# Performance work log

Hardware: AMD Instinct MI355X
Metric: run time of the kernel (lower is better)

The kernel has to match this reference:

```python
import jax, jax.numpy as jnp
import numpy as np

B, S, D = 2, 2048, 2048
H, KVH = 32, 8
HD = D // H            # 64
G = H // KVH           # 4 kv groups
SCALE = 1.0 / np.sqrt(HD)


def setup_inputs() -> dict:
    key = jax.random.key(0)
    k1, k2, k3, k4, k5 = jax.random.split(key, 5)
    hidden_states = jax.random.normal(k1, (B, S, D), dtype=jnp.float32)
    Wq = jax.random.normal(k2, (D, H * HD), dtype=jnp.float32) * 0.02
    Wk = jax.random.normal(k3, (D, KVH * HD), dtype=jnp.float32) * 0.02
    Wv = jax.random.normal(k4, (D, KVH * HD), dtype=jnp.float32) * 0.02
    Wo = jax.random.normal(k5, (H * HD, D), dtype=jnp.float32) * 0.02
    return {"hidden_states": hidden_states, "Wq": Wq, "Wk": Wk, "Wv": Wv, "Wo": Wo}


def reference(hidden_states, Wq, Wk, Wv, Wo):
    B_, S_, _ = hidden_states.shape
    q = (hidden_states @ Wq).reshape(B_, S_, H, HD).transpose(0, 2, 1, 3)      # [B,H,S,HD]
    k = (hidden_states @ Wk).reshape(B_, S_, KVH, HD).transpose(0, 2, 1, 3)    # [B,KVH,S,HD]
    v = (hidden_states @ Wv).reshape(B_, S_, KVH, HD).transpose(0, 2, 1, 3)
    # repeat_interleave over head dim: kv head g serves q heads [g*G, (g+1)*G)
    k = jnp.repeat(k, G, axis=1)  # [B,H,S,HD]
    v = jnp.repeat(v, G, axis=1)
    scores = jnp.einsum('bhqd,bhkd->bhqk', q, k) * SCALE
    probs = jax.nn.softmax(scores.astype(jnp.float32), axis=-1).astype(q.dtype)
    # dropout is identity in eval mode
    out = jnp.einsum('bhqk,bhkd->bhqd', probs, v)             # [B,H,S,HD]
    out = out.transpose(0, 2, 1, 3).reshape(B_, S_, H * HD)   # [B,S,D]
    return out @ Wo
```

## Files before the change

kernel.cpp:

```cpp
#include <hip/hip_runtime.h>
#include <hip/hip_bf16.h>

typedef unsigned short u16;
typedef __attribute__((ext_vector_type(8))) short short8;
typedef __attribute__((ext_vector_type(4))) float f32x4;
typedef __attribute__((ext_vector_type(16))) float f32x16;
typedef __attribute__((ext_vector_type(4))) unsigned short u16x4;
typedef __attribute__((ext_vector_type(4))) int int4v;

#define S_LEN 2048
#define NH 32
#define NKV 8
#define QSCALE 0.18033688011112042f
#define PSHIFT 14.0f

__device__ __forceinline__ float fexp2(float x) { return __builtin_amdgcn_exp2f(x); }

__device__ __forceinline__ u16 f2bf(float f) {
  unsigned int u = __builtin_bit_cast(unsigned int, f);
  u += 0x7fffu + ((u >> 16) & 1u);
  return (u16)(u >> 16);
}

__device__ __forceinline__ unsigned int pk2bf(float a, float b) {
  float2 t; t.x = a; t.y = b;
  __hip_bfloat162 h = __float22bfloat162_rn(t);
  unsigned int r;
  __builtin_memcpy(&r, &h, 4);
  return r;
}

__device__ __forceinline__ void async16(const void* g, void* l) {
  __builtin_amdgcn_global_load_lds(
      (__attribute__((address_space(1))) void*)g,
      (__attribute__((address_space(3))) void*)l, 16, 0, 0);
}

__device__ __forceinline__ short8 mk_pf(unsigned a, unsigned b, unsigned c, unsigned d) {
  int4v t; t.x = (int)a; t.y = (int)b; t.z = (int)c; t.w = (int)d;
  return __builtin_bit_cast(short8, t);
}

__global__ __launch_bounds__(256) void prep_kernel(const float* __restrict__ X,
                                                   const float* __restrict__ Wq,
                                                   const float* __restrict__ Wk,
                                                   const float* __restrict__ Wv,
                                                   const float* __restrict__ Wo,
                                                   u16* __restrict__ Xb,
                                                   u16* __restrict__ Wqt,
                                                   u16* __restrict__ Wkt,
                                                   u16* __restrict__ Wvt,
                                                   u16* __restrict__ Wot) {
  __shared__ float tile[32][33];
  int bx = blockIdx.x, tid = threadIdx.x;
  if (bx < 8192) {
    int idx = bx * 256 + tid;
    float4 v = ((const float4*)X)[idx];
    u16x4 o;
    o.x = f2bf(v.x); o.y = f2bf(v.y); o.z = f2bf(v.z); o.w = f2bf(v.w);
    *(u16x4*)&Xb[(size_t)idx * 4] = o;
    return;
  }
  const float* in; u16* out; int N, bi;
  if (bx < 12288)      { bi = bx - 8192;  in = Wq; out = Wqt; N = 2048; }
  else if (bx < 13312) { bi = bx - 12288; in = Wk; out = Wkt; N = 512; }
  else if (bx < 14336) { bi = bx - 13312; in = Wv; out = Wvt; N = 512; }
  else                 { bi = bx - 14336; in = Wo; out = Wot; N = 2048; }
  const int K = 2048;
  int nbx = N >> 5;
  int n0 = (bi % nbx) * 32, k0 = (bi / nbx) * 32;
  int tx = tid & 31, ty = tid >> 5;
#pragma unroll
  for (int i = 0; i < 32; i += 8)
    tile[ty + i][tx] = in[(size_t)(k0 + ty + i) * N + n0 + tx];
  __syncthreads();
#pragma unroll
  for (int i = 0; i < 32; i += 8)
    out[(size_t)(n0 + ty + i) * K + k0 + tx] = f2bf(tile[tx][ty + i]);
}

__global__ __launch_bounds__(256) void gemm_qkv(const u16* __restrict__ A,
                                                const u16* __restrict__ Wqt,
                                                const u16* __restrict__ Wkvt,
                                                u16* __restrict__ Qb,
                                                u16* __restrict__ KVb) {
  __shared__ u16 la0[4096], la1[4096], lb0[4096], lb1[4096];
  int tid = threadIdx.x, bx = blockIdx.x;
  int mode, bm, bn;
  const u16* Bt;
  if (bx < 512) { mode = 0; bm = bx >> 4; bn = bx & 15; Bt = Wqt; }
  else          { mode = 1; int b2 = bx - 512; bm = b2 >> 3; bn = b2 & 7; Bt = Wkvt; }
  const int K = 2048;
  int w = tid >> 6, lane = tid & 63, qd = lane >> 4, ln = lane & 15;
  int wm = w >> 1, wn = w & 1;
  f32x4 acc[4][4];
#pragma unroll
  for (int i = 0; i < 4; ++i)
#pragma unroll
    for (int j = 0; j < 4; ++j) acc[i][j] = {0.f, 0.f, 0.f, 0.f};

  const u16* Ab = A + (size_t)bm * 128 * K;
  const u16* Bb = Bt + (size_t)bn * 128 * K;
  int row0 = tid >> 2, c0 = tid & 3;
  int g0 = c0 ^ (row0 & 3) ^ ((row0 >> 2) & 3);
  int s1 = tid + 256, row1 = s1 >> 2, c1 = s1 & 3;
  int g1 = c1 ^ (row1 & 3) ^ ((row1 >> 2) & 3);
  int pat = (ln & 3) ^ ((ln >> 2) & 3);
  int goff = (qd ^ pat) * 8;
  const u16* pa0 = Ab + (size_t)row0 * K + g0 * 8;
  const u16* pa1 = Ab + (size_t)row1 * K + g1 * 8;
  const u16* pb0 = Bb + (size_t)row0 * K + g0 * 8;
  const u16* pb1 = Bb + (size_t)row1 * K + g1 * 8;

#define QKV_STAGE(LA, LB, OFS)                      \
  async16(pa0 + (OFS), &LA[tid * 8]);               \
  async16(pa1 + (OFS), &LA[2048 + tid * 8]);        \
  async16(pb0 + (OFS), &LB[tid * 8]);               \
  async16(pb1 + (OFS), &LB[2048 + tid * 8]);

#define QKV_COMPUTE(LA, LB)                                                        \
  {                                                                                \
    short8 af[4], bf[4];                                                           \
    _Pragma("unroll") for (int i = 0; i < 4; ++i)                                  \
        af[i] = *(const short8*)&LA[(wm * 64 + i * 16 + ln) * 32 + goff];          \
    _Pragma("unroll") for (int j = 0; j < 4; ++j)                                  \
        bf[j] = *(const short8*)&LB[(wn * 64 + j * 16 + ln) * 32 + goff];          \
    __builtin_amdgcn_s_setprio(1);                                                 \
    _Pragma("unroll") for (int i = 0; i < 4; ++i)                                  \
      _Pragma("unroll") for (int j = 0; j < 4; ++j)                                \
        acc[i][j] =                                                                \
            __builtin_amdgcn_mfma_f32_16x16x32_bf16(af[i], bf[j], acc[i][j], 0, 0, 0); \
    __builtin_amdgcn_s_setprio(0);                                                 \
  }

  QKV_STAGE(la0, lb0, 0);
  __syncthreads();

  for (int kt = 0; kt < K; kt += 64) {
    QKV_STAGE(la1, lb1, kt + 32);
    QKV_COMPUTE(la0, lb0);
    __syncthreads();
    if (kt + 64 < K) { QKV_STAGE(la0, lb0, kt + 64); }
    QKV_COMPUTE(la1, lb1);
    __syncthreads();
  }
#undef QKV_STAGE
#undef QKV_COMPUTE

#pragma unroll
  for (int i = 0; i < 4; ++i)
#pragma unroll
    for (int r = 0; r < 4; ++r) {
      int m = bm * 128 + wm * 64 + i * 16 + qd * 4 + r;
      int b = m >> 11, s = m & 2047;
#pragma unroll
      for (int j = 0; j < 4; ++j) {
        int n = bn * 128 + wn * 64 + j * 16 + ln;
        float v = acc[i][j][r];
        int hh = n >> 6, hd = n & 63;
        if (mode == 0) {
          Qb[(((size_t)(b * NH + hh)) * S_LEN + s) * 64 + hd] = f2bf(v * QSCALE);
        } else {
          if (hh < 8)
            KVb[(((size_t)(b * NKV + hh)) * S_LEN + s) * 64 + hd] = f2bf(v);
          else
            KVb[2097152 + (((size_t)(b * NKV + (hh - 8))) * 64 + hd) * S_LEN + s] = f2bf(v);
        }
      }
    }
}

__global__ __launch_bounds__(256) void gemm_out(const u16* __restrict__ A,
                                                const u16* __restrict__ Bt,
                                                float* __restrict__ outp) {
  __shared__ u16 la0[4096], la1[4096], lb0[4096], lb1[4096];
  const int K = 2048, N = 2048;
  int tid = threadIdx.x;
  int bm = blockIdx.x >> 4, bn = blockIdx.x & 15;
  int w = tid >> 6, lane = tid & 63, qd = lane >> 4, ln = lane & 15;
  int wm = w >> 1, wn = w & 1;
  f32x4 acc[4][4];
#pragma unroll
  for (int i = 0; i < 4; ++i)
#pragma unroll
    for (int j = 0; j < 4; ++j) acc[i][j] = {0.f, 0.f, 0.f, 0.f};

  const u16* Ab = A + (size_t)bm * 128 * K;
  const u16* Bb = Bt + (size_t)bn * 128 * K;
  int row0 = tid >> 2, c0 = tid & 3;
  int g0 = c0 ^ (row0 & 3) ^ ((row0 >> 2) & 3);
  int s1 = tid + 256, row1 = s1 >> 2, c1 = s1 & 3;
  int g1 = c1 ^ (row1 & 3) ^ ((row1 >> 2) & 3);
  int pat = (ln & 3) ^ ((ln >> 2) & 3);
  int goff = (qd ^ pat) * 8;
  const u16* pa0 = Ab + (size_t)row0 * K + g0 * 8;
  const u16* pa1 = Ab + (size_t)row1 * K + g1 * 8;
  const u16* pb0 = Bb + (size_t)row0 * K + g0 * 8;
  const u16* pb1 = Bb + (size_t)row1 * K + g1 * 8;

#define OUT_STAGE(LA, LB, OFS)                      \
  async16(pa0 + (OFS), &LA[tid * 8]);               \
  async16(pa1 + (OFS), &LA[2048 + tid * 8]);        \
  async16(pb0 + (OFS), &LB[tid * 8]);               \
  async16(pb1 + (OFS), &LB[2048 + tid * 8]);

#define OUT_COMPUTE(LA, LB)                                                        \
  {                                                                                \
    short8 af[4], bf[4];                                                           \
    _Pragma("unroll") for (int i = 0; i < 4; ++i)                                  \
        af[i] = *(const short8*)&LA[(wm * 64 + i * 16 + ln) * 32 + goff];          \
    _Pragma("unroll") for (int j = 0; j < 4; ++j)                                  \
        bf[j] = *(const short8*)&LB[(wn * 64 + j * 16 + ln) * 32 + goff];          \
    __builtin_amdgcn_s_setprio(1);                                                 \
    _Pragma("unroll") for (int i = 0; i < 4; ++i)                                  \
      _Pragma("unroll") for (int j = 0; j < 4; ++j)                                \
        acc[i][j] =                                                                \
            __builtin_amdgcn_mfma_f32_16x16x32_bf16(af[i], bf[j], acc[i][j], 0, 0, 0); \
    __builtin_amdgcn_s_setprio(0);                                                 \
  }

  OUT_STAGE(la0, lb0, 0);
  __syncthreads();

  for (int kt = 0; kt < K; kt += 64) {
    OUT_STAGE(la1, lb1, kt + 32);
    OUT_COMPUTE(la0, lb0);
    __syncthreads();
    if (kt + 64 < K) { OUT_STAGE(la0, lb0, kt + 64); }
    OUT_COMPUTE(la1, lb1);
    __syncthreads();
  }
#undef OUT_STAGE
#undef OUT_COMPUTE

#pragma unroll
  for (int i = 0; i < 4; ++i)
#pragma unroll
    for (int r = 0; r < 4; ++r) {
      int m = bm * 128 + wm * 64 + i * 16 + qd * 4 + r;
#pragma unroll
      for (int j = 0; j < 4; ++j) {
        int n = bn * 128 + wn * 64 + j * 16 + ln;
        outp[(size_t)m * N + n] = acc[i][j][r];
      }
    }
}

__global__ __launch_bounds__(256, 2) void attn_kernel(const u16* __restrict__ Q,
                                                      const u16* __restrict__ K,
                                                      const u16* __restrict__ VT,
                                                      u16* __restrict__ Ao) {
  __shared__ u16 sh[16384];
  int tid = threadIdx.x;
  int w = tid >> 6, lane = tid & 63;
  int l31 = lane & 31, l5 = lane >> 5;
  int qt = blockIdx.x & 7, bh = blockIdx.x >> 3;
  int b = bh >> 5, h = bh & 31, g = h >> 2;
  const u16* gQ = Q + ((size_t)bh * S_LEN + qt * 256) * 64;
  const u16* gK = K + (size_t)(b * NKV + g) * S_LEN * 64;
  const u16* gV = VT + (size_t)(b * NKV + g) * 64 * S_LEN;

  int p7 = l31 & 7;

  int s0 = tid, r0 = s0 >> 3, c0 = s0 & 7, gg0 = c0 ^ (r0 & 7);
  int s1 = tid + 256, r1 = s1 >> 3, c1 = s1 & 7, gg1 = c1 ^ (r1 & 7);

#pragma unroll
  for (int k = 0; k < 8; ++k) {
    int s = tid + k * 256;
    int q = s >> 3, c = s & 7, gg = c ^ (q & 7);
    async16(gQ + (size_t)q * 64 + gg * 8, &sh[s * 8]);
  }
  __syncthreads();
  short8 qf[2][4];
#pragma unroll
  for (int qg = 0; qg < 2; ++qg) {
    int qrow = w * 64 + qg * 32 + l31;
#pragma unroll
    for (int ks = 0; ks < 4; ++ks)
      qf[qg][ks] = *(const short8*)&sh[qrow * 64 + ((ks * 2 + l5) ^ p7) * 8];
  }
  __syncthreads();

  async16(gK + (size_t)r0 * 64 + gg0 * 8, &sh[s0 * 8]);
  async16(gK + (size_t)r1 * 64 + gg1 * 8, &sh[s1 * 8]);
  async16(gV + (size_t)r0 * S_LEN + gg0 * 8, &sh[8192 + s0 * 8]);
  async16(gV + (size_t)r1 * S_LEN + gg1 * 8, &sh[8192 + s1 * 8]);
  __syncthreads();

  const f32x16 psh16 = {-PSHIFT, -PSHIFT, -PSHIFT, -PSHIFT, -PSHIFT, -PSHIFT,
                        -PSHIFT, -PSHIFT, -PSHIFT, -PSHIFT, -PSHIFT, -PSHIFT,
                        -PSHIFT, -PSHIFT, -PSHIFT, -PSHIFT};
  f32x16 accA0, accA1, accB0, accB1;
#pragma unroll
  for (int t = 0; t < 16; ++t) { accA0[t] = 0.f; accA1[t] = 0.f; accB0[t] = 0.f; accB1[t] = 0.f; }
  float liA = 0.f, liB = 0.f;

#define SOFTMAX32(SC, LI, PF0, PF1)                                              \
  short8 PF0, PF1;                                                               \
  {                                                                              \
    float p[16];                                                                 \
    _Pragma("unroll") for (int t = 0; t < 16; ++t) p[t] = fexp2(SC[t]);          \
    _Pragma("unroll") for (int t = 0; t < 16; t += 4)                            \
        LI += (p[t] + p[t + 1]) + (p[t + 2] + p[t + 3]);                         \
    unsigned W[8];                                                               \
    _Pragma("unroll") for (int t = 0; t < 8; ++t) W[t] = pk2bf(p[2 * t], p[2 * t + 1]); \
    auto ra = __builtin_amdgcn_permlane32_swap((int)W[0], (int)W[2], false, false); \
    auto rb = __builtin_amdgcn_permlane32_swap((int)W[1], (int)W[3], false, false); \
    auto rc = __builtin_amdgcn_permlane32_swap((int)W[4], (int)W[6], false, false); \
    auto rd = __builtin_amdgcn_permlane32_swap((int)W[5], (int)W[7], false, false); \
    PF0 = mk_pf((unsigned)ra[0], (unsigned)rb[0], (unsigned)ra[1], (unsigned)rb[1]); \
    PF1 = mk_pf((unsigned)rc[0], (unsigned)rd[0], (unsigned)rc[1], (unsigned)rd[1]); \
  }

  for (int c = 0; c < 32; ++c) {
    int cur = c & 1;
    if (c < 31) {
      int nb = cur ^ 1, cn = c + 1;
      async16(gK + (size_t)(cn * 64 + r0) * 64 + gg0 * 8, &sh[nb * 4096 + s0 * 8]);
      async16(gK + (size_t)(cn * 64 + r1) * 64 + gg1 * 8, &sh[nb * 4096 + s1 * 8]);
      async16(gV + (size_t)r0 * S_LEN + cn * 64 + gg0 * 8, &sh[8192 + nb * 4096 + s0 * 8]);
      async16(gV + (size_t)r1 * S_LEN + cn * 64 + gg1 * 8, &sh[8192 + nb * 4096 + s1 * 8]);
    }
    const u16* kb = &sh[cur * 4096];
    const u16* vb = &sh[8192 + cur * 4096];

#pragma unroll
    for (int kblk = 0; kblk < 2; ++kblk) {
      f32x16 scA = psh16, scB = psh16;
      __builtin_amdgcn_s_setprio(1);
#pragma unroll
      for (int ks = 0; ks < 4; ++ks) {
        short8 kf = *(const short8*)&kb[(kblk * 32 + l31) * 64 + ((ks * 2 + l5) ^ p7) * 8];
        scA = __builtin_amdgcn_mfma_f32_32x32x16_bf16(kf, qf[0][ks], scA, 0, 0, 0);
        scB = __builtin_amdgcn_mfma_f32_32x32x16_bf16(kf, qf[1][ks], scB, 0, 0, 0);
      }
      __builtin_amdgcn_s_setprio(0);

      SOFTMAX32(scA, liA, pfA0, pfA1)
      SOFTMAX32(scB, liB, pfB0, pfB1)

      __builtin_amdgcn_s_setprio(1);
#pragma unroll
      for (int hb = 0; hb < 2; ++hb) {
        short8 vf = *(const short8*)&vb[(hb * 32 + l31) * 64 + ((kblk * 4 + l5) ^ p7) * 8];
        if (hb == 0) {
          accA0 = __builtin_amdgcn_mfma_f32_32x32x16_bf16(vf, pfA0, accA0, 0, 0, 0);
          accB0 = __builtin_amdgcn_mfma_f32_32x32x16_bf16(vf, pfB0, accB0, 0, 0, 0);
        } else {
          accA1 = __builtin_amdgcn_mfma_f32_32x32x16_bf16(vf, pfA0, accA1, 0, 0, 0);
          accB1 = __builtin_amdgcn_mfma_f32_32x32x16_bf16(vf, pfB0, accB1, 0, 0, 0);
        }
      }
#pragma unroll
      for (int hb = 0; hb < 2; ++hb) {
        short8 vf = *(const short8*)&vb[(hb * 32 + l31) * 64 + ((kblk * 4 + 2 + l5) ^ p7) * 8];
        if (hb == 0) {
          accA0 = __builtin_amdgcn_mfma_f32_32x32x16_bf16(vf, pfA1, accA0, 0, 0, 0);
          accB0 = __builtin_amdgcn_mfma_f32_32x32x16_bf16(vf, pfB1, accB0, 0, 0, 0);
        } else {
          accA1 = __builtin_amdgcn_mfma_f32_32x32x16_bf16(vf, pfA1, accA1, 0, 0, 0);
          accB1 = __builtin_amdgcn_mfma_f32_32x32x16_bf16(vf, pfB1, accB1, 0, 0, 0);
        }
      }
      __builtin_amdgcn_s_setprio(0);
    }
    __syncthreads();
  }
#undef SOFTMAX32

  {
    float l = liA + __shfl_xor(liA, 32);
    float inv = 1.f / l;
    int q = qt * 256 + w * 64 + l31;
    size_t base = ((size_t)b * S_LEN + q) * 2048 + h * 64;
#pragma unroll
    for (int rq = 0; rq < 4; ++rq) {
      u16x4 o0, o1;
#pragma unroll
      for (int rr = 0; rr < 4; ++rr) {
        o0[rr] = f2bf(accA0[rq * 4 + rr] * inv);
        o1[rr] = f2bf(accA1[rq * 4 + rr] * inv);
      }
      *(u16x4*)&Ao[base + rq * 8 + l5 * 4] = o0;
      *(u16x4*)&Ao[base + 32 + rq * 8 + l5 * 4] = o1;
    }
  }
  {
    float l = liB + __shfl_xor(liB, 32);
    float inv = 1.f / l;
    int q = qt * 256 + w * 64 + 32 + l31;
    size_t base = ((size_t)b * S_LEN + q) * 2048 + h * 64;
#pragma unroll
    for (int rq = 0; rq < 4; ++rq) {
      u16x4 o0, o1;
#pragma unroll
      for (int rr = 0; rr < 4; ++rr) {
        o0[rr] = f2bf(accB0[rq * 4 + rr] * inv);
        o1[rr] = f2bf(accB1[rq * 4 + rr] * inv);
      }
      *(u16x4*)&Ao[base + rq * 8 + l5 * 4] = o0;
      *(u16x4*)&Ao[base + 32 + rq * 8 + l5 * 4] = o1;
    }
  }
}

extern "C" void kernel_launch(void* const* d_in, const int* in_sizes, int n_in,
                              void* d_out, int out_size, void* d_ws, size_t ws_size,
                              hipStream_t stream) {
  const float* X  = (const float*)d_in[0];
  const float* Wq = (const float*)d_in[1];
  const float* Wk = (const float*)d_in[2];
  const float* Wv = (const float*)d_in[3];
  const float* Wo = (const float*)d_in[4];
  char* ws = (char*)d_ws;
  u16* Xb  = (u16*)(ws);
  u16* Wqt = (u16*)(ws + 16777216);
  u16* Wkt = (u16*)(ws + 25165824);
  u16* Wvt = (u16*)(ws + 27262976);
  u16* Wot = (u16*)(ws + 29360128);
  u16* Qb  = (u16*)(ws + 37748736);
  u16* Kb  = (u16*)(ws + 54525952);
  u16* VTb = (u16*)(ws + 58720256);
  u16* Ab  = (u16*)(ws + 62914560);
  float* out = (float*)d_out;

  prep_kernel<<<18432, 256, 0, stream>>>(X, Wq, Wk, Wv, Wo, Xb, Wqt, Wkt, Wvt, Wot);
  gemm_qkv<<<768, 256, 0, stream>>>(Xb, Wqt, Wkt, Qb, Kb);
  attn_kernel<<<512, 256, 0, stream>>>(Qb, Kb, VTb, Ab);
  gemm_out<<<512, 256, 0, stream>>>(Ab, Wot, out);
}
```

Before: 304.0 us.

## Triple-buffer LDS stages in QKV and output GEMMs with explicit vmcnt waits

Replaces the double-buffered K loop in both projection GEMMs with a three-stage LDS ring. Two tiles are kept in flight, and partial s_waitcnt vmcnt counts with raw barriers replace the full __syncthreads. The aim is to hide global-load latency behind MFMA work, since only the oldest stage now has to land before compute. The cost is 50% more shared memory per block, which may reduce occupancy, and hand-tuned waitcnt values that depend on the async16 instruction count per stage.

```diff
diff --git a/kernel.cpp b/kernel.cpp
--- a/kernel.cpp
+++ b/kernel.cpp
@@ -84,7 +84,8 @@
                                                 const u16* __restrict__ Wkvt,
                                                 u16* __restrict__ Qb,
                                                 u16* __restrict__ KVb) {
-  __shared__ u16 la0[4096], la1[4096], lb0[4096], lb1[4096];
+  __shared__ u16 la0[4096], la1[4096], la2[4096];
+  __shared__ u16 lb0[4096], lb1[4096], lb2[4096];
   int tid = threadIdx.x, bx = blockIdx.x;
   int mode, bm, bn;
   const u16* Bt;
@@ -133,19 +134,38 @@
     __builtin_amdgcn_s_setprio(0);                                                 \
   }
 
+#define QKV_STEP(CA, CB, SA, SB, SOFS, VM)                          \
+  asm volatile("s_waitcnt lgkmcnt(0)" ::: "memory");                \
+  __builtin_amdgcn_s_barrier();                                     \
+  QKV_STAGE(SA, SB, SOFS);                                          \
+  asm volatile("s_waitcnt vmcnt(" #VM ")" ::: "memory");            \
+  __builtin_amdgcn_s_barrier();                                     \
+  QKV_COMPUTE(CA, CB);
+
+#define QKV_STEP_T(CA, CB, VM)                                      \
+  asm volatile("s_waitcnt lgkmcnt(0)" ::: "memory");                \
+  __builtin_amdgcn_s_barrier();                                     \
+  asm volatile("s_waitcnt vmcnt(" #VM ")" ::: "memory");            \
+  __builtin_amdgcn_s_barrier();                                     \
+  QKV_COMPUTE(CA, CB);
+
   QKV_STAGE(la0, lb0, 0);
-  __syncthreads();
-
-  for (int kt = 0; kt < K; kt += 64) {
-    QKV_STAGE(la1, lb1, kt + 32);
-    QKV_COMPUTE(la0, lb0);
-    __syncthreads();
-    if (kt + 64 < K) { QKV_STAGE(la0, lb0, kt + 64); }
-    QKV_COMPUTE(la1, lb1);
-    __syncthreads();
-  }
+  QKV_STAGE(la1, lb1, 32);
+
+  for (int t3 = 0; t3 < 60; t3 += 3) {
+    int ofs = t3 * 32;
+    QKV_STEP(la0, lb0, la2, lb2, ofs + 64, 8);
+    QKV_STEP(la1, lb1, la0, lb0, ofs + 96, 8);
+    QKV_STEP(la2, lb2, la1, lb1, ofs + 128, 8);
+  }
+  QKV_STEP(la0, lb0, la2, lb2, 1984, 8);
+  QKV_STEP(la1, lb1, la0, lb0, 2016, 8);
+  QKV_STEP_T(la2, lb2, 4);
+  QKV_STEP_T(la0, lb0, 0);
 #undef QKV_STAGE
 #undef QKV_COMPUTE
+#undef QKV_STEP
+#undef QKV_STEP_T
 
 #pragma unroll
   for (int i = 0; i < 4; ++i)
@@ -173,7 +193,8 @@
 __global__ __launch_bounds__(256) void gemm_out(const u16* __restrict__ A,
                                                 const u16* __restrict__ Bt,
                                                 float* __restrict__ outp) {
-  __shared__ u16 la0[4096], la1[4096], lb0[4096], lb1[4096];
+  __shared__ u16 la0[4096], la1[4096], la2[4096];
+  __shared__ u16 lb0[4096], lb1[4096], lb2[4096];
   const int K = 2048, N = 2048;
   int tid = threadIdx.x;
   int bm = blockIdx.x >> 4, bn = blockIdx.x & 15;
@@ -219,19 +240,38 @@
     __builtin_amdgcn_s_setprio(0);                                                 \
   }
 
+#define OUT_STEP(CA, CB, SA, SB, SOFS, VM)                          \
+  asm volatile("s_waitcnt lgkmcnt(0)" ::: "memory");                \
+  __builtin_amdgcn_s_barrier();                                     \
+  OUT_STAGE(SA, SB, SOFS);                                          \
+  asm volatile("s_waitcnt vmcnt(" #VM ")" ::: "memory");            \
+  __builtin_amdgcn_s_barrier();                                     \
+  OUT_COMPUTE(CA, CB);
+
+#define OUT_STEP_T(CA, CB, VM)                                      \
+  asm volatile("s_waitcnt lgkmcnt(0)" ::: "memory");                \
+  __builtin_amdgcn_s_barrier();                                     \
+  asm volatile("s_waitcnt vmcnt(" #VM ")" ::: "memory");            \
+  __builtin_amdgcn_s_barrier();                                     \
+  OUT_COMPUTE(CA, CB);
+
   OUT_STAGE(la0, lb0, 0);
-  __syncthreads();
-
-  for (int kt = 0; kt < K; kt += 64) {
-    OUT_STAGE(la1, lb1, kt + 32);
-    OUT_COMPUTE(la0, lb0);
-    __syncthreads();
-    if (kt + 64 < K) { OUT_STAGE(la0, lb0, kt + 64); }
-    OUT_COMPUTE(la1, lb1);
-    __syncthreads();
-  }
+  OUT_STAGE(la1, lb1, 32);
+
+  for (int t3 = 0; t3 < 60; t3 += 3) {
+    int ofs = t3 * 32;
+    OUT_STEP(la0, lb0, la2, lb2, ofs + 64, 8);
+    OUT_STEP(la1, lb1, la0, lb0, ofs + 96, 8);
+    OUT_STEP(la2, lb2, la1, lb1, ofs + 128, 8);
+  }
+  OUT_STEP(la0, lb0, la2, lb2, 1984, 8);
+  OUT_STEP(la1, lb1, la0, lb0, 2016, 8);
+  OUT_STEP_T(la2, lb2, 4);
+  OUT_STEP_T(la0, lb0, 0);
 #undef OUT_STAGE
 #undef OUT_COMPUTE
+#undef OUT_STEP
+#undef OUT_STEP_T
 
 #pragma unroll
   for (int i = 0; i < 4; ++i)
```

After: 327.7 us. 1.08x slower.
